# Kernel optimization log

Hardware: AMD Instinct MI355X
Metric: run time of the kernel (lower is better)

## Reference

```python
import jax, jax.numpy as jnp
import numpy as np

B, T_IN, F, NB = 32768, 3, 6, 10
H = 256
BD = H // 2            # baseline_dim
T_OUT = 5
DIN = F + H + BD       # decoder LSTMCell input size
EPS = 1e-5


def _lstm_cell(x, h, c, W_ih, W_hh, b_ih, b_hh):
    # PyTorch gate order: i, f, g, o
    z = x @ W_ih.T + h @ W_hh.T + b_ih + b_hh
    i, f, g, o = jnp.split(z, 4, axis=-1)
    c = jax.nn.sigmoid(f) * c + jax.nn.sigmoid(i) * jnp.tanh(g)
    h = jax.nn.sigmoid(o) * jnp.tanh(c)
    return h, c


def _lstm_layer(xs, W_ih, W_hh, b_ih, b_hh):
    # xs: (T, B, D_in) -> outputs (T, B, H), final (h, c)
    Bn = xs.shape[1]
    h0 = jnp.zeros((Bn, H), xs.dtype)
    c0 = jnp.zeros((Bn, H), xs.dtype)

    def step(carry, x):
        h, c = carry
        h, c = _lstm_cell(x, h, c, W_ih, W_hh, b_ih, b_hh)
        return (h, c), h

    (hT, cT), ys = jax.lax.scan(step, (h0, c0), xs)
    return ys, hT, cT


def setup_inputs() -> dict:
    key = jax.random.key(0)
    ks = jax.random.split(key, 16)
    s = 0.05
    d = {
        "cbc_input": jax.random.normal(ks[0], (B, T_IN, F), jnp.float32),
        "baseline": jax.random.normal(ks[1], (B, NB), jnp.float32),
        # encoder LSTM layer 0 / 1
        "W_ih0": jax.random.normal(ks[2], (4 * H, F), jnp.float32) * s,
        "W_hh0": jax.random.normal(ks[3], (4 * H, H), jnp.float32) * s,
        "b_ih0": jnp.zeros((4 * H,), jnp.float32),
        "b_hh0": jnp.zeros((4 * H,), jnp.float32),
        "W_ih1": jax.random.normal(ks[4], (4 * H, H), jnp.float32) * s,
        "W_hh1": jax.random.normal(ks[5], (4 * H, H), jnp.float32) * s,
        "b_ih1": jnp.zeros((4 * H,), jnp.float32),
        "b_hh1": jnp.zeros((4 * H,), jnp.float32),
        # baseline encoder: Linear + ReLU + LayerNorm
        "Wb": jax.random.normal(ks[6], (BD, NB), jnp.float32) * s,
        "bb": jnp.zeros((BD,), jnp.float32),
        "ln_g": jnp.ones((BD,), jnp.float32),
        "ln_b": jnp.zeros((BD,), jnp.float32),
        # Bahdanau attention
        "W1a": jax.random.normal(ks[7], (H, H), jnp.float32) * s,
        "b1a": jnp.zeros((H,), jnp.float32),
        "W2a": jax.random.normal(ks[8], (H, H), jnp.float32) * s,
        "b2a": jnp.zeros((H,), jnp.float32),
        "va": jax.random.normal(ks[9], (1, H), jnp.float32) * s,
        "ba": jnp.zeros((1,), jnp.float32),
        # decoder LSTMCell
        "Wd_ih": jax.random.normal(ks[10], (4 * H, DIN), jnp.float32) * s,
        "Wd_hh": jax.random.normal(ks[11], (4 * H, H), jnp.float32) * s,
        "bd_ih": jnp.zeros((4 * H,), jnp.float32),
        "bd_hh": jnp.zeros((4 * H,), jnp.float32),
        # output projection MLP
        "Wo1": jax.random.normal(ks[12], (BD, H), jnp.float32) * s,
        "bo1": jnp.zeros((BD,), jnp.float32),
        "Wo2": jax.random.normal(ks[13], (F, BD), jnp.float32) * s,
        "bo2": jnp.zeros((F,), jnp.float32),
    }
    return d


def reference(cbc_input, baseline, W_ih0, W_hh0, b_ih0, b_hh0,
              W_ih1, W_hh1, b_ih1, b_hh1, Wb, bb, ln_g, ln_b,
              W1a, b1a, W2a, b2a, va, ba,
              Wd_ih, Wd_hh, bd_ih, bd_hh, Wo1, bo1, Wo2, bo2):
    # ---- encoder (2-layer LSTM, batch_first; eval mode so no dropout) ----
    xs = jnp.swapaxes(cbc_input, 0, 1)                      # (T, B, F)
    y0, _, _ = _lstm_layer(xs, W_ih0, W_hh0, b_ih0, b_hh0)  # (T, B, H)
    y1, hT, cT = _lstm_layer(y0, W_ih1, W_hh1, b_ih1, b_hh1)
    encoder_outputs = jnp.swapaxes(y1, 0, 1)                # (B, T, H)

    # ---- baseline encoder: Linear -> ReLU -> LayerNorm ----
    z = jax.nn.relu(baseline @ Wb.T + bb)
    mu = jnp.mean(z, axis=-1, keepdims=True)
    var = jnp.mean((z - mu) ** 2, axis=-1, keepdims=True)
    baseline_repr = (z - mu) * jax.lax.rsqrt(var + EPS) * ln_g + ln_b  # (B, BD)

    enc_proj = encoder_outputs @ W2a.T + b2a                # (B, T, H) precomputed
    last_cbc0 = cbc_input[:, -1, :]                         # (B, F)

    def step(carry, _):
        h, c, last_cbc = carry
        # Bahdanau attention
        q = (h @ W1a.T + b1a)[:, None, :]                   # (B, 1, H)
        scores = jnp.tanh(q + enc_proj) @ va.T + ba         # (B, T, 1)
        weights = jax.nn.softmax(scores, axis=1)
        context = jnp.sum(weights * encoder_outputs, axis=1)  # (B, H)
        dec_in = jnp.concatenate([last_cbc, context, baseline_repr], axis=1)
        h, c = _lstm_cell(dec_in, h, c, Wd_ih, Wd_hh, bd_ih, bd_hh)
        delta = jax.nn.relu(h @ Wo1.T + bo1) @ Wo2.T + bo2
        pred = last_cbc + delta
        return (h, c, pred), pred

    _, preds = jax.lax.scan(step, (hT, cT, last_cbc0), None, length=T_OUT)
    return jnp.swapaxes(preds, 0, 1)                        # (B, 5, F)
```

## Files before the change

### kernel.cpp

```cpp
#include <hip/hip_runtime.h>

typedef unsigned short u16;
typedef __bf16 bf16x8 __attribute__((ext_vector_type(8)));
typedef float f32x4 __attribute__((ext_vector_type(4)));

#define BATCH 32768L

__device__ __forceinline__ u16 f2b(float f) {
  union { float f; unsigned int u; } v; v.f = f;
  unsigned int r = v.u + 0x7fffu + ((v.u >> 16) & 1u);
  return (u16)(r >> 16);
}
__device__ __forceinline__ float b2f(u16 h) {
  union { unsigned int u; float f; } v; v.u = ((unsigned int)h) << 16;
  return v.f;
}
__device__ __forceinline__ float rcpf(float x) { return __builtin_amdgcn_rcpf(x); }
__device__ __forceinline__ float sigf(float x) {
  return rcpf(1.f + __builtin_amdgcn_exp2f(-1.442695041f * x));
}
__device__ __forceinline__ float tanh_f(float x) {
  return 1.f - 2.f * rcpf(1.f + __builtin_amdgcn_exp2f(2.885390082f * x));
}

__device__ __forceinline__ void gload16(const void* g, void* l) {
  __builtin_amdgcn_global_load_lds((const __attribute__((address_space(1))) unsigned int*)g,
                                   (__attribute__((address_space(3))) unsigned int*)l,
                                   16, 0, 0);
}

struct PrepP {
  const float* s[9]; u16* d[9]; int sc[9]; int dc[9]; long n[9];
  const float* ba[3]; const float* bb_[3]; float* bo[3];
};

__global__ void prep_kernel(PrepP p, long cvtTotal, long total) {
  for (long i = (long)blockIdx.x * blockDim.x + threadIdx.x; i < total;
       i += (long)gridDim.x * blockDim.x) {
    if (i < cvtTotal) {
      long off = i; int sg = 0;
      while (off >= p.n[sg]) { off -= p.n[sg]; ++sg; }
      long r = off / p.dc[sg]; int c = (int)(off - r * p.dc[sg]);
      p.d[sg][off] = (c < p.sc[sg]) ? f2b(p.s[sg][r * (long)p.sc[sg] + c]) : (u16)0;
    } else {
      long j = i - cvtTotal; int sg = (int)(j >> 10); int k = (int)(j & 1023);
      p.bo[sg][k] = p.ba[sg][k] + p.bb_[sg][k];
    }
  }
}

template <int EPI, int NG, int REMAP, int MINW>
__global__ __launch_bounds__(256, MINW)
void mfma_gemm7(const u16* __restrict__ A1, long lda1, int K1,
                const u16* __restrict__ W1, int wld1,
                const u16* __restrict__ A2, long lda2, int K2,
                const u16* __restrict__ W2, int wld2,
                int gs, int ys, const float* __restrict__ bias,
                u16* __restrict__ out0, int ldo, int relu,
                const float* __restrict__ cprev, float* __restrict__ cout,
                u16* __restrict__ hout, int ldh)
{
  __shared__ u16 As[2][64 * 32];
  __shared__ u16 Bs[2][NG * 64 * 32];
  const int tid = threadIdx.x;
  const int l = tid & 63, w = tid >> 6;

  int row_blk, yb;
  if constexpr (REMAP) {
    const int vid = blockIdx.x;
    row_blk = (vid >> 5) * 8 + (vid & 7);
    yb = (vid >> 3) & 3;
  } else {
    row_blk = blockIdx.x;
    yb = blockIdx.y;
  }
  const long bm = (long)row_blk * 64;

  const int nch1 = K1 >> 5;
  const int nch2 = A2 ? (K2 >> 5) : 0;
  const int nt = nch1 + nch2;

  const int colb = l & 15, rq = l >> 4;

  f32x4 acc[4][NG];
  {
    float bw[NG];
#pragma unroll
    for (int g = 0; g < NG; ++g) bw[g] = bias[g * gs + yb * ys + w * 16 + colb];
#pragma unroll
    for (int rf = 0; rf < 4; ++rf)
#pragma unroll
      for (int g = 0; g < NG; ++g) acc[rf][g] = (f32x4){bw[g], bw[g], bw[g], bw[g]};
  }

  const int l4q = l >> 2;
  const int swzs = (((l & 3) - (l >> 3)) & 3) * 16;

  const char* pA;
  const char* pB[NG];
  auto initA = [&](const u16* A, long lda) {
    pA = (const char*)A + ((bm + w * 16 + l4q) * lda) * 2 + swzs;
  };
  auto initB = [&](const u16* W, int wld) {
#pragma unroll
    for (int c = 0; c < NG; ++c) {
      const int brow = (w * NG + c) * 16 + l4q;
      const long wrow = (long)(brow >> 6) * gs + (long)yb * ys + (brow & 63);
      pB[c] = (const char*)W + (wrow * (long)wld) * 2 + swzs;
    }
  };
  auto stage = [&](int buf) {
    gload16(pA, &As[buf][(w * 16) * 32]);
    pA += 64;
#pragma unroll
    for (int c = 0; c < NG; ++c) {
      gload16(pB[c], &Bs[buf][((w * NG + c) * 16) * 32]);
      pB[c] += 64;
    }
  };

  initA(A1, lda1);
  initB(W1, wld1);
  stage(0);

  const int rb = l & 15;
  const int koff = ((((l >> 4) + ((l & 15) >> 1)) & 3) * 8);
  int cur = 0;
  for (int ch = 0; ch < nt; ++ch) {
    __syncthreads();
    if (ch + 1 < nt) {
      if (A2 && ch + 1 == nch1) { initA(A2, lda2); initB(W2, wld2); }
      stage(cur ^ 1);
    }
    const u16* Ab = As[cur];
    const u16* Bb = Bs[cur];
    bf16x8 af[4];
#pragma unroll
    for (int rf = 0; rf < 4; ++rf)
      af[rf] = *(const bf16x8*)&Ab[(rf * 16 + rb) * 32 + koff];
#pragma unroll
    for (int g = 0; g < NG; ++g) {
      bf16x8 bfr = *(const bf16x8*)&Bb[(g * 64 + w * 16 + rb) * 32 + koff];
#pragma unroll
      for (int rf = 0; rf < 4; ++rf)
        acc[rf][g] = __builtin_amdgcn_mfma_f32_16x16x32_bf16(af[rf], bfr, acc[rf][g], 0, 0, 0);
    }
    cur ^= 1;
  }

  if constexpr (EPI == 0) {
#pragma unroll
    for (int g = 0; g < NG; ++g) {
      const int wrow = g * gs + yb * ys + w * 16 + colb;
#pragma unroll
      for (int rf = 0; rf < 4; ++rf) {
#pragma unroll
        for (int r = 0; r < 4; ++r) {
          float vv = acc[rf][g][r];
          if (relu) vv = fmaxf(vv, 0.f);
          out0[(bm + rf * 16 + rq * 4 + r) * (long)ldo + wrow] = f2b(vv);
        }
      }
    }
  } else {
    const int cb = yb * ys + w * 16 + colb;
#pragma unroll
    for (int rf = 0; rf < 4; ++rf) {
#pragma unroll
      for (int r = 0; r < 4; ++r) {
        const long row = bm + rf * 16 + rq * 4 + r;
        const float zi = acc[rf][0][r];
        const float zf = acc[rf][1][r];
        const float zg = acc[rf][2][r];
        const float zo = acc[rf][3][r];
        const float cp = cprev ? cprev[row * 256 + cb] : 0.f;
        const float cn = sigf(zf) * cp + sigf(zi) * tanh_f(zg);
        const float hn = sigf(zo) * tanh_f(cn);
        cout[row * 256 + cb] = cn;
        hout[row * (long)ldh + cb] = f2b(hn);
      }
    }
  }
}

__global__ __launch_bounds__(256, 2)
void qattn_kernel(const u16* __restrict__ A1, long lda1,
                  const u16* __restrict__ W1, int wld1,
                  const float* __restrict__ bias,
                  const u16* __restrict__ ep, const u16* __restrict__ eo,
                  const float* __restrict__ va, const float* __restrict__ ba,
                  u16* __restrict__ dec_in)
{
  __shared__ u16 As[2][64 * 32];
  __shared__ u16 Bs[2][4 * 64 * 32];
  __shared__ u16 qs[64 * 260];
  const int tid = threadIdx.x;
  const int l = tid & 63, w = tid >> 6;
  const long bm = (long)blockIdx.x * 64;
  const int nt = 8;

  const int colb = l & 15, rq = l >> 4;

  f32x4 acc[4][4];
  {
    float bw[4];
#pragma unroll
    for (int g = 0; g < 4; ++g) bw[g] = bias[g * 64 + w * 16 + colb];
#pragma unroll
    for (int rf = 0; rf < 4; ++rf)
#pragma unroll
      for (int g = 0; g < 4; ++g) acc[rf][g] = (f32x4){bw[g], bw[g], bw[g], bw[g]};
  }

  const int l4q = l >> 2;
  const int swzs = (((l & 3) - (l >> 3)) & 3) * 16;

  const char* pA = (const char*)A1 + ((bm + w * 16 + l4q) * lda1) * 2 + swzs;
  const char* pB[4];
#pragma unroll
  for (int c = 0; c < 4; ++c) {
    const int brow = (w * 4 + c) * 16 + l4q;
    pB[c] = (const char*)W1 + ((long)brow * wld1) * 2 + swzs;
  }
  auto stage = [&](int buf) {
    gload16(pA, &As[buf][(w * 16) * 32]);
    pA += 64;
#pragma unroll
    for (int c = 0; c < 4; ++c) {
      gload16(pB[c], &Bs[buf][((w * 4 + c) * 16) * 32]);
      pB[c] += 64;
    }
  };

  stage(0);
  const int rb = l & 15;
  const int koff = ((((l >> 4) + ((l & 15) >> 1)) & 3) * 8);
  int cur = 0;
  for (int ch = 0; ch < nt; ++ch) {
    __syncthreads();
    if (ch + 1 < nt) stage(cur ^ 1);
    const u16* Ab = As[cur];
    const u16* Bb = Bs[cur];
    bf16x8 af[4];
#pragma unroll
    for (int rf = 0; rf < 4; ++rf)
      af[rf] = *(const bf16x8*)&Ab[(rf * 16 + rb) * 32 + koff];
#pragma unroll
    for (int g = 0; g < 4; ++g) {
      bf16x8 bfr = *(const bf16x8*)&Bb[(g * 64 + w * 16 + rb) * 32 + koff];
#pragma unroll
      for (int rf = 0; rf < 4; ++rf)
        acc[rf][g] = __builtin_amdgcn_mfma_f32_16x16x32_bf16(af[rf], bfr, acc[rf][g], 0, 0, 0);
    }
    cur ^= 1;
  }

#pragma unroll
  for (int g = 0; g < 4; ++g) {
    const int col = g * 64 + w * 16 + colb;
#pragma unroll
    for (int rf = 0; rf < 4; ++rf)
#pragma unroll
      for (int r = 0; r < 4; ++r)
        qs[(rf * 16 + rq * 4 + r) * 260 + col] = f2b(acc[rf][g][r]);
  }
  __syncthreads();

  const float ba0 = ba[0];
  const int c = l * 4;
  float vav[4];
  {
    float4 vv = *(const float4*)&va[c];
    vav[0] = vv.x; vav[1] = vv.y; vav[2] = vv.z; vav[3] = vv.w;
  }
  for (int rr = 0; rr < 16; ++rr) {
    const int lrow = w * 16 + rr;
    const long row = bm + lrow;
    float qv[4];
    {
      ushort4 qu = *(const ushort4*)&qs[lrow * 260 + c];
      qv[0] = b2f(qu.x); qv[1] = b2f(qu.y); qv[2] = b2f(qu.z); qv[3] = b2f(qu.w);
    }
    float s[3];
#pragma unroll
    for (int t = 0; t < 3; ++t) {
      ushort4 eu = *(const ushort4*)&ep[row * 768 + t * 256 + c];
      float p = tanh_f(qv[0] + b2f(eu.x)) * vav[0]
              + tanh_f(qv[1] + b2f(eu.y)) * vav[1]
              + tanh_f(qv[2] + b2f(eu.z)) * vav[2]
              + tanh_f(qv[3] + b2f(eu.w)) * vav[3];
#pragma unroll
      for (int m = 32; m; m >>= 1) p += __shfl_xor(p, m);
      s[t] = p + ba0;
    }
    const float mx = fmaxf(s[0], fmaxf(s[1], s[2]));
    const float e0 = __expf(s[0] - mx), e1 = __expf(s[1] - mx), e2 = __expf(s[2] - mx);
    const float inv = rcpf(e0 + e1 + e2);
    const float w0 = e0 * inv, w1 = e1 * inv, w2 = e2 * inv;
    const ushort4 a0 = *(const ushort4*)&eo[row * 768 + 0 * 256 + c];
    const ushort4 a1 = *(const ushort4*)&eo[row * 768 + 1 * 256 + c];
    const ushort4 a2 = *(const ushort4*)&eo[row * 768 + 2 * 256 + c];
    u16* dp = &dec_in[row * 416 + 6 + c];
    dp[0] = f2b(w0 * b2f(a0.x) + w1 * b2f(a1.x) + w2 * b2f(a2.x));
    dp[1] = f2b(w0 * b2f(a0.y) + w1 * b2f(a1.y) + w2 * b2f(a2.y));
    dp[2] = f2b(w0 * b2f(a0.z) + w1 * b2f(a1.z) + w2 * b2f(a2.z));
    dp[3] = f2b(w0 * b2f(a0.w) + w1 * b2f(a1.w) + w2 * b2f(a2.w));
  }
}

__global__ __launch_bounds__(256, 2)
void t1delta_kernel(const u16* __restrict__ A1, long lda1,
                    const u16* __restrict__ W1, int wld1,
                    const float* __restrict__ bias,
                    const float* __restrict__ Wo2, const float* __restrict__ bo2,
                    const float* __restrict__ lastp, int lstride,
                    float* __restrict__ outp, int ostride,
                    u16* __restrict__ dec_in)
{
  __shared__ u16 As[2][64 * 32];
  __shared__ u16 Bs[2][2 * 64 * 32];
  __shared__ u16 t1s[64 * 136];
  __shared__ float w2s[768];
  __shared__ float part[64][4][6];
  const int tid = threadIdx.x;
  const int l = tid & 63, w = tid >> 6;
  const long bm = (long)blockIdx.x * 64;
  const int nt = 8;

  for (int i = tid; i < 768; i += 256) w2s[i] = Wo2[i];

  const int colb = l & 15, rq = l >> 4;

  f32x4 acc[4][2];
  {
    float bw[2];
#pragma unroll
    for (int g = 0; g < 2; ++g) bw[g] = bias[g * 64 + w * 16 + colb];
#pragma unroll
    for (int rf = 0; rf < 4; ++rf)
#pragma unroll
      for (int g = 0; g < 2; ++g) acc[rf][g] = (f32x4){bw[g], bw[g], bw[g], bw[g]};
  }

  const int l4q = l >> 2;
  const int swzs = (((l & 3) - (l >> 3)) & 3) * 16;

  const char* pA = (const char*)A1 + ((bm + w * 16 + l4q) * lda1) * 2 + swzs;
  const char* pB[2];
#pragma unroll
  for (int c = 0; c < 2; ++c) {
    const int brow = (w * 2 + c) * 16 + l4q;
    pB[c] = (const char*)W1 + ((long)brow * wld1) * 2 + swzs;
  }
  auto stage = [&](int buf) {
    gload16(pA, &As[buf][(w * 16) * 32]);
    pA += 64;
#pragma unroll
    for (int c = 0; c < 2; ++c) {
      gload16(pB[c], &Bs[buf][((w * 2 + c) * 16) * 32]);
      pB[c] += 64;
    }
  };

  stage(0);
  const int rb = l & 15;
  const int koff = ((((l >> 4) + ((l & 15) >> 1)) & 3) * 8);
  int cur = 0;
  for (int ch = 0; ch < nt; ++ch) {
    __syncthreads();
    if (ch + 1 < nt) stage(cur ^ 1);
    const u16* Ab = As[cur];
    const u16* Bb = Bs[cur];
    bf16x8 af[4];
#pragma unroll
    for (int rf = 0; rf < 4; ++rf)
      af[rf] = *(const bf16x8*)&Ab[(rf * 16 + rb) * 32 + koff];
#pragma unroll
    for (int g = 0; g < 2; ++g) {
      bf16x8 bfr = *(const bf16x8*)&Bb[(g * 64 + w * 16 + rb) * 32 + koff];
#pragma unroll
      for (int rf = 0; rf < 4; ++rf)
        acc[rf][g] = __builtin_amdgcn_mfma_f32_16x16x32_bf16(af[rf], bfr, acc[rf][g], 0, 0, 0);
    }
    cur ^= 1;
  }

#pragma unroll
  for (int g = 0; g < 2; ++g) {
    const int col = g * 64 + w * 16 + colb;
#pragma unroll
    for (int rf = 0; rf < 4; ++rf)
#pragma unroll
      for (int r = 0; r < 4; ++r)
        t1s[(rf * 16 + rq * 4 + r) * 136 + col] = f2b(fmaxf(acc[rf][g][r], 0.f));
  }
  __syncthreads();

  const int rw = tid >> 2, q = tid & 3;
  float p[6] = {0.f, 0.f, 0.f, 0.f, 0.f, 0.f};
  const u16* tp = &t1s[rw * 136 + q * 32];
#pragma unroll
  for (int it = 0; it < 4; ++it) {
    int4 chunk = *(const int4*)&tp[it * 8];
    const u16* cu = (const u16*)&chunk;
#pragma unroll
    for (int e = 0; e < 8; ++e) {
      const float tv = b2f(cu[e]);
      const int k = q * 32 + it * 8 + e;
#pragma unroll
      for (int j = 0; j < 6; ++j) p[j] += tv * w2s[j * 128 + k];
    }
  }
#pragma unroll
  for (int j = 0; j < 6; ++j) part[rw][q][j] = p[j];
  __syncthreads();
  if (tid < 64) {
    const long r2 = bm + tid;
#pragma unroll
    for (int j = 0; j < 6; ++j) {
      const float d = bo2[j] + part[tid][0][j] + part[tid][1][j] + part[tid][2][j] + part[tid][3][j];
      const float pr = lastp[r2 * lstride + j] + d;
      outp[r2 * ostride + j] = pr;
      dec_in[r2 * 416 + j] = f2b(pr);
    }
  }
}

__global__ __launch_bounds__(256)
void front_kernel(const float* __restrict__ cbc, const float* __restrict__ baseline,
                  const float* __restrict__ Wb, const float* __restrict__ bb,
                  const float* __restrict__ ln_g, const float* __restrict__ ln_b,
                  u16* __restrict__ dec_in, u16* __restrict__ xbf)
{
  __shared__ float wbs[1280];
  __shared__ float bbs[128], lgs[128], lbs[128];
  const int tid = threadIdx.x;
  for (int i = tid; i < 1280; i += 256) wbs[i] = Wb[i];
  if (tid < 128) { bbs[tid] = bb[tid]; lgs[tid] = ln_g[tid]; lbs[tid] = ln_b[tid]; }
  __syncthreads();
  const int l = tid & 63, w = tid >> 6;
  const long row = (long)blockIdx.x * 4 + w;
#pragma unroll
  for (int e = l; e < 96; e += 64) {
    const int t = e >> 5, c = e & 31;
    xbf[(row * 3 + t) * 32 + c] = (c < 6) ? f2b(cbc[row * 18 + t * 6 + c]) : (u16)0;
  }
  if (l < 6) dec_in[row * 416 + l] = f2b(cbc[row * 18 + 12 + l]);
  else if (l < 32) dec_in[row * 416 + 390 + (l - 6)] = 0;
  float bl[10];
#pragma unroll
  for (int k = 0; k < 10; ++k) bl[k] = baseline[row * 10 + k];
  const int c0 = l, c1 = l + 64;
  float z0 = bbs[c0], z1 = bbs[c1];
#pragma unroll
  for (int k = 0; k < 10; ++k) { z0 += bl[k] * wbs[c0 * 10 + k]; z1 += bl[k] * wbs[c1 * 10 + k]; }
  z0 = fmaxf(z0, 0.f); z1 = fmaxf(z1, 0.f);
  float s = z0 + z1, sq = z0 * z0 + z1 * z1;
#pragma unroll
  for (int m = 32; m; m >>= 1) { s += __shfl_xor(s, m); sq += __shfl_xor(sq, m); }
  const float mu = s * (1.f / 128.f);
  const float var = sq * (1.f / 128.f) - mu * mu;
  const float rs = rsqrtf(var + 1e-5f);
  dec_in[row * 416 + 262 + c0] = f2b((z0 - mu) * rs * lgs[c0] + lbs[c0]);
  dec_in[row * 416 + 262 + c1] = f2b((z1 - mu) * rs * lgs[c1] + lbs[c1]);
}

extern "C" void kernel_launch(void* const* d_in, const int* in_sizes, int n_in,
                              void* d_out, int out_size, void* d_ws, size_t ws_size,
                              hipStream_t stream) {
  const float* cbc   = (const float*)d_in[0];
  const float* base  = (const float*)d_in[1];
  const float* W_ih0 = (const float*)d_in[2];
  const float* W_hh0 = (const float*)d_in[3];
  const float* b_ih0 = (const float*)d_in[4];
  const float* b_hh0 = (const float*)d_in[5];
  const float* W_ih1 = (const float*)d_in[6];
  const float* W_hh1 = (const float*)d_in[7];
  const float* b_ih1 = (const float*)d_in[8];
  const float* b_hh1 = (const float*)d_in[9];
  const float* Wb    = (const float*)d_in[10];
  const float* bb    = (const float*)d_in[11];
  const float* ln_g  = (const float*)d_in[12];
  const float* ln_b  = (const float*)d_in[13];
  const float* W1a   = (const float*)d_in[14];
  const float* b1a   = (const float*)d_in[15];
  const float* W2a   = (const float*)d_in[16];
  const float* b2a   = (const float*)d_in[17];
  const float* va    = (const float*)d_in[18];
  const float* ba    = (const float*)d_in[19];
  const float* Wd_ih = (const float*)d_in[20];
  const float* Wd_hh = (const float*)d_in[21];
  const float* bd_ih = (const float*)d_in[22];
  const float* bd_hh = (const float*)d_in[23];
  const float* Wo1   = (const float*)d_in[24];
  const float* bo1   = (const float*)d_in[25];
  const float* Wo2   = (const float*)d_in[26];
  const float* bo2   = (const float*)d_in[27];
  float* out = (float*)d_out;
  (void)in_sizes; (void)n_in; (void)out_size;

  unsigned char* wsb = (unsigned char*)d_ws;
  size_t off = 0;
  auto alloc = [&](size_t bytes) -> void* {
    void* p = wsb + off;
    off += (bytes + 255) & ~(size_t)255;
    return p;
  };
  u16* wih0b = (u16*)alloc(1024 * 32 * 2);
  u16* whh0b = (u16*)alloc(1024 * 256 * 2);
  u16* wih1b = (u16*)alloc(1024 * 256 * 2);
  u16* whh1b = (u16*)alloc(1024 * 256 * 2);
  u16* wdihb = (u16*)alloc(1024 * 416 * 2);
  u16* wdhhb = (u16*)alloc(1024 * 256 * 2);
  u16* w1ab  = (u16*)alloc(256 * 256 * 2);
  u16* w2ab  = (u16*)alloc(256 * 256 * 2);
  u16* wo1b  = (u16*)alloc(128 * 256 * 2);
  float* bsum0 = (float*)alloc(1024 * 4);
  float* bsum1 = (float*)alloc(1024 * 4);
  float* bsumd = (float*)alloc(1024 * 4);

  const long perRow = 6656;
  long avail = (long)ws_size - (long)off - 32768;
  long R = avail > 0 ? avail / perRow : 512;
  R &= ~511L;
  if (R > BATCH) R = BATCH;
  if (R < 512) R = 512;

  u16* xbf    = (u16*)alloc((size_t)R * 96 * 2);
  u16* y0     = (u16*)alloc((size_t)R * 768 * 2);
  u16* y1     = (u16*)alloc((size_t)R * 768 * 2);
  float* cbuf = (float*)alloc((size_t)R * 256 * 4);
  u16* hdec0  = (u16*)alloc((size_t)R * 256 * 2);
  u16* hdec1  = (u16*)alloc((size_t)R * 256 * 2);
  u16* qt1    = (u16*)alloc((size_t)R * 256 * 2);
  u16* dec_in = (u16*)alloc((size_t)R * 416 * 2);
  (void)qt1;

  {
    PrepP p;
    const float* ss[9] = {W_ih0, W_hh0, W_ih1, W_hh1, Wd_ih, Wd_hh, W1a, W2a, Wo1};
    u16* dd[9]         = {wih0b, whh0b, wih1b, whh1b, wdihb, wdhhb, w1ab, w2ab, wo1b};
    int scv[9]         = {6, 256, 256, 256, 390, 256, 256, 256, 256};
    int dcv[9]         = {32, 256, 256, 256, 416, 256, 256, 256, 256};
    long rows[9]       = {1024, 1024, 1024, 1024, 1024, 1024, 256, 256, 128};
    long cvtTotal = 0;
    for (int i = 0; i < 9; ++i) {
      p.s[i] = ss[i]; p.d[i] = dd[i]; p.sc[i] = scv[i]; p.dc[i] = dcv[i];
      p.n[i] = rows[i] * dcv[i]; cvtTotal += p.n[i];
    }
    p.ba[0] = b_ih0; p.bb_[0] = b_hh0; p.bo[0] = bsum0;
    p.ba[1] = b_ih1; p.bb_[1] = b_hh1; p.bo[1] = bsum1;
    p.ba[2] = bd_ih; p.bb_[2] = bd_hh; p.bo[2] = bsumd;
    prep_kernel<<<dim3(2048), dim3(256), 0, stream>>>(p, cvtTotal, cvtTotal + 3072);
  }

  const dim3 blk(256);

  for (long r0 = 0; r0 < BATCH; r0 += R) {
    const long Rc = (BATCH - r0 < R) ? (BATCH - r0) : R;
    const unsigned nb = (unsigned)(Rc / 64);
    const dim3 gcell(nb * 4);
    const float* cbc_c  = cbc + r0 * 18;
    const float* base_c = base + r0 * 10;
    float* out_c = out + r0 * 30;

    front_kernel<<<dim3((unsigned)(Rc / 4)), blk, 0, stream>>>(
        cbc_c, base_c, Wb, bb, ln_g, ln_b, dec_in, xbf);

    for (int t = 0; t < 3; ++t) {
      const u16* a2 = t ? (y0 + (t - 1) * 256) : nullptr;
      mfma_gemm7<1, 4, 1, 4><<<gcell, blk, 0, stream>>>(
          xbf + t * 32, 96, 32, wih0b, 32,
          a2, 768, 256, whh0b, 256,
          256, 64, bsum0,
          nullptr, 0, 0,
          (t ? cbuf : nullptr), cbuf, y0 + t * 256, 768);
    }
    for (int t = 0; t < 3; ++t) {
      const u16* a2 = t ? (y1 + (t - 1) * 256) : nullptr;
      mfma_gemm7<1, 4, 1, 4><<<gcell, blk, 0, stream>>>(
          y0 + t * 256, 768, 256, wih1b, 256,
          a2, 768, 256, whh1b, 256,
          256, 64, bsum1,
          nullptr, 0, 0,
          (t ? cbuf : nullptr), cbuf, y1 + t * 256, 768);
    }
    mfma_gemm7<0, 4, 0, 3><<<dim3(nb * 3, 1), blk, 0, stream>>>(
        y1, 256, 256, w2ab, 256,
        nullptr, 0, 0, nullptr, 0,
        64, 0, b2a,
        y0, 256, 0,
        nullptr, nullptr, nullptr, 0);

    const u16* hcur = y1 + 2 * 256; long hld = 768;
    for (int s = 0; s < 5; ++s) {
      qattn_kernel<<<dim3(nb), blk, 0, stream>>>(
          hcur, hld, w1ab, 256, b1a, y0, y1, va, ba, dec_in);
      u16* hnext = (s & 1) ? hdec1 : hdec0;
      mfma_gemm7<1, 4, 1, 4><<<gcell, blk, 0, stream>>>(
          dec_in, 416, 416, wdihb, 416,
          hcur, hld, 256, wdhhb, 256,
          256, 64, bsumd,
          nullptr, 0, 0,
          cbuf, cbuf, hnext, 256);
      hcur = hnext; hld = 256;
      const float* lastp = (s == 0) ? (cbc_c + 12) : (out_c + (long)(s - 1) * 6);
      const int lstr = (s == 0) ? 18 : 30;
      t1delta_kernel<<<dim3(nb), blk, 0, stream>>>(
          hcur, 256, wo1b, 256, bo1,
          Wo2, bo2, lastp, lstr, out_c + (long)s * 6, 30, dec_in);
    }
  }
}
```

Baseline: 881.6 us.

## Add dedicated 128-row LSTM cell GEMM with triple-buffered LDS pipeline

New measurement: 842.4 us. 1.05x faster.

```diff
diff --git a/kernel.cpp b/kernel.cpp
--- a/kernel.cpp
+++ b/kernel.cpp
@@ -45,6 +45,135 @@
     } else {
       long j = i - cvtTotal; int sg = (int)(j >> 10); int k = (int)(j & 1023);
       p.bo[sg][k] = p.ba[sg][k] + p.bb_[sg][k];
+    }
+  }
+}
+
+__global__ __launch_bounds__(256, 2)
+void cell_gemm(const u16* __restrict__ A1, long lda1, int K1,
+               const u16* __restrict__ W1, int wld1,
+               const u16* __restrict__ A2, long lda2, int K2,
+               const u16* __restrict__ W2, int wld2,
+               const float* __restrict__ bias,
+               const float* __restrict__ cprev, float* __restrict__ cout,
+               u16* __restrict__ hout, int ldh)
+{
+  __shared__ u16 As[3][128 * 32];
+  __shared__ u16 Bs[3][256 * 32];
+  const int tid = threadIdx.x;
+  const int l = tid & 63, w = tid >> 6;
+  const int vid = blockIdx.x;
+  const int rbk = (vid >> 5) * 8 + (vid & 7);
+  const int yb = (vid >> 3) & 3;
+  const long bm = (long)rbk * 128;
+
+  const int nch1 = K1 >> 5;
+  const int nch2 = A2 ? (K2 >> 5) : 0;
+  const int nt = nch1 + nch2;
+
+  const int colb = l & 15, rq = l >> 4;
+  const int cb = yb * 64 + w * 16 + colb;
+
+  f32x4 acc[8][4];
+  {
+    float bw[4];
+#pragma unroll
+    for (int g = 0; g < 4; ++g) bw[g] = bias[g * 256 + cb];
+#pragma unroll
+    for (int rf = 0; rf < 8; ++rf)
+#pragma unroll
+      for (int g = 0; g < 4; ++g) acc[rf][g] = (f32x4){bw[g], bw[g], bw[g], bw[g]};
+  }
+
+  const int srow = tid >> 2;
+  const int srcu = (((tid & 3) - (tid >> 3)) & 3) * 16;
+
+  const char* pA0; const char* pA1_;
+  const char* pB[4];
+  auto initAp = [&](const u16* A, long lda) {
+    pA0  = (const char*)A + ((bm + srow) * lda) * 2 + srcu;
+    pA1_ = (const char*)A + ((bm + 64 + srow) * lda) * 2 + srcu;
+  };
+  auto initBp = [&](const u16* W, int wld) {
+#pragma unroll
+    for (int j = 0; j < 4; ++j) {
+      const long wrow = (long)(tid >> 6) * 256 + yb * 64 + j * 16 + ((tid >> 2) & 15);
+      pB[j] = (const char*)W + (wrow * (long)wld) * 2 + srcu;
+    }
+  };
+  auto issueA = [&](int s, int sl) {
+    if (s == nch1) initAp(A2, lda2);
+    gload16(pA0, &As[sl][w * 512]); pA0 += 64;
+    gload16(pA1_, &As[sl][2048 + w * 512]); pA1_ += 64;
+  };
+  auto issueB = [&](int s, int sl) {
+    if (s == nch1) initBp(W2, wld2);
+#pragma unroll
+    for (int j = 0; j < 4; ++j) {
+      gload16(pB[j], &Bs[sl][j * 2048 + w * 512]); pB[j] += 64;
+    }
+  };
+
+  initAp(A1, lda1);
+  initBp(W1, wld1);
+  issueA(0, 0); issueB(0, 0);
+  if (nt > 1) { issueA(1, 1); issueB(1, 1); }
+
+  const int rb = l & 15;
+  const int koff = (((l >> 4) + ((l & 15) >> 1)) & 3) * 8;
+  int slot = 0;
+  for (int ch = 0; ch < nt; ++ch) {
+    if (ch + 1 < nt) {
+      asm volatile("s_waitcnt vmcnt(6)\n\ts_barrier" ::: "memory");
+    } else {
+      asm volatile("s_waitcnt vmcnt(0)\n\ts_barrier" ::: "memory");
+    }
+    const int nsl = (slot + 2 >= 3) ? slot - 1 : slot + 2;
+    const u16* Ab = As[slot];
+    const u16* Bb = Bs[slot];
+    bf16x8 af[8];
+#pragma unroll
+    for (int rf = 0; rf < 8; ++rf)
+      af[rf] = *(const bf16x8*)&Ab[(rf * 16 + rb) * 32 + koff];
+    bf16x8 bf0 = *(const bf16x8*)&Bb[(w * 64 + rb) * 32 + koff];
+    bf16x8 bf1 = *(const bf16x8*)&Bb[(w * 64 + 16 + rb) * 32 + koff];
+    if (ch + 2 < nt) issueA(ch + 2, nsl);
+    __builtin_amdgcn_s_setprio(1);
+#pragma unroll
+    for (int rf = 0; rf < 8; ++rf)
+      acc[rf][0] = __builtin_amdgcn_mfma_f32_16x16x32_bf16(af[rf], bf0, acc[rf][0], 0, 0, 0);
+#pragma unroll
+    for (int rf = 0; rf < 8; ++rf)
+      acc[rf][1] = __builtin_amdgcn_mfma_f32_16x16x32_bf16(af[rf], bf1, acc[rf][1], 0, 0, 0);
+    __builtin_amdgcn_s_setprio(0);
+    bf16x8 bf2 = *(const bf16x8*)&Bb[(w * 64 + 32 + rb) * 32 + koff];
+    bf16x8 bf3 = *(const bf16x8*)&Bb[(w * 64 + 48 + rb) * 32 + koff];
+    if (ch + 2 < nt) issueB(ch + 2, nsl);
+    __builtin_amdgcn_s_setprio(1);
+#pragma unroll
+    for (int rf = 0; rf < 8; ++rf)
+      acc[rf][2] = __builtin_amdgcn_mfma_f32_16x16x32_bf16(af[rf], bf2, acc[rf][2], 0, 0, 0);
+#pragma unroll
+    for (int rf = 0; rf < 8; ++rf)
+      acc[rf][3] = __builtin_amdgcn_mfma_f32_16x16x32_bf16(af[rf], bf3, acc[rf][3], 0, 0, 0);
+    __builtin_amdgcn_s_setprio(0);
+    slot = (slot + 1 == 3) ? 0 : slot + 1;
+  }
+
+#pragma unroll
+  for (int rf = 0; rf < 8; ++rf) {
+#pragma unroll
+    for (int r = 0; r < 4; ++r) {
+      const long row = bm + rf * 16 + rq * 4 + r;
+      const float zi = acc[rf][0][r];
+      const float zf = acc[rf][1][r];
+      const float zg = acc[rf][2][r];
+      const float zo = acc[rf][3][r];
+      const float cp = cprev ? cprev[row * 256 + cb] : 0.f;
+      const float cn = sigf(zf) * cp + sigf(zi) * tanh_f(zg);
+      const float hn = sigf(zo) * tanh_f(cn);
+      cout[row * 256 + cb] = cn;
+      hout[row * (long)ldh + cb] = f2b(hn);
     }
   }
 }
@@ -521,10 +650,10 @@
 
   const long perRow = 6656;
   long avail = (long)ws_size - (long)off - 32768;
-  long R = avail > 0 ? avail / perRow : 512;
-  R &= ~511L;
+  long R = avail > 0 ? avail / perRow : 1024;
+  R &= ~1023L;
   if (R > BATCH) R = BATCH;
-  if (R < 512) R = 512;
+  if (R < 1024) R = 1024;
 
   u16* xbf    = (u16*)alloc((size_t)R * 96 * 2);
   u16* y0     = (u16*)alloc((size_t)R * 768 * 2);
@@ -532,9 +661,7 @@
   float* cbuf = (float*)alloc((size_t)R * 256 * 4);
   u16* hdec0  = (u16*)alloc((size_t)R * 256 * 2);
   u16* hdec1  = (u16*)alloc((size_t)R * 256 * 2);
-  u16* qt1    = (u16*)alloc((size_t)R * 256 * 2);
   u16* dec_in = (u16*)alloc((size_t)R * 416 * 2);
-  (void)qt1;
 
   {
     PrepP p;
@@ -558,8 +685,9 @@
 
   for (long r0 = 0; r0 < BATCH; r0 += R) {
     const long Rc = (BATCH - r0 < R) ? (BATCH - r0) : R;
-    const unsigned nb = (unsigned)(Rc / 64);
-    const dim3 gcell(nb * 4);
+    const unsigned nb64 = (unsigned)(Rc / 64);
+    const unsigned nb128 = (unsigned)(Rc / 128);
+    const dim3 gcell(nb128 * 4);
     const float* cbc_c  = cbc + r0 * 18;
     const float* base_c = base + r0 * 10;
     float* out_c = out + r0 * 30;
@@ -569,23 +697,21 @@
 
     for (int t = 0; t < 3; ++t) {
       const u16* a2 = t ? (y0 + (t - 1) * 256) : nullptr;
-      mfma_gemm7<1, 4, 1, 4><<<gcell, blk, 0, stream>>>(
+      cell_gemm<<<gcell, blk, 0, stream>>>(
           xbf + t * 32, 96, 32, wih0b, 32,
           a2, 768, 256, whh0b, 256,
-          256, 64, bsum0,
-          nullptr, 0, 0,
+          bsum0,
           (t ? cbuf : nullptr), cbuf, y0 + t * 256, 768);
     }
     for (int t = 0; t < 3; ++t) {
       const u16* a2 = t ? (y1 + (t - 1) * 256) : nullptr;
-      mfma_gemm7<1, 4, 1, 4><<<gcell, blk, 0, stream>>>(
+      cell_gemm<<<gcell, blk, 0, stream>>>(
           y0 + t * 256, 768, 256, wih1b, 256,
           a2, 768, 256, whh1b, 256,
-          256, 64, bsum1,
-          nullptr, 0, 0,
+          bsum1,
           (t ? cbuf : nullptr), cbuf, y1 + t * 256, 768);
     }
-    mfma_gemm7<0, 4, 0, 3><<<dim3(nb * 3, 1), blk, 0, stream>>>(
+    mfma_gemm7<0, 4, 0, 3><<<dim3(nb64 * 3, 1), blk, 0, stream>>>(
         y1, 256, 256, w2ab, 256,
         nullptr, 0, 0, nullptr, 0,
         64, 0, b2a,
@@ -594,19 +720,18 @@
 
     const u16* hcur = y1 + 2 * 256; long hld = 768;
     for (int s = 0; s < 5; ++s) {
-      qattn_kernel<<<dim3(nb), blk, 0, stream>>>(
+      qattn_kernel<<<dim3(nb64), blk, 0, stream>>>(
           hcur, hld, w1ab, 256, b1a, y0, y1, va, ba, dec_in);
       u16* hnext = (s & 1) ? hdec1 : hdec0;
-      mfma_gemm7<1, 4, 1, 4><<<gcell, blk, 0, stream>>>(
+      cell_gemm<<<gcell, blk, 0, stream>>>(
           dec_in, 416, 416, wdihb, 416,
           hcur, hld, 256, wdhhb, 256,
-          256, 64, bsumd,
-          nullptr, 0, 0,
+          bsumd,
           cbuf, cbuf, hnext, 256);
       hcur = hnext; hld = 256;
       const float* lastp = (s == 0) ? (cbc_c + 12) : (out_c + (long)(s - 1) * 6);
       const int lstr = (s == 0) ? 18 : 30;
-      t1delta_kernel<<<dim3(nb), blk, 0, stream>>>(
+      t1delta_kernel<<<dim3(nb64), blk, 0, stream>>>(
           hcur, 256, wo1b, 256, bo1,
           Wo2, bo2, lastp, lstr, out_c + (long)s * 6, 30, dec_in);
     }
```
